# Performance work log

Hardware: AMD Instinct MI355X
Metric: run time of the kernel (lower is better)

Reference implementation:

```python
import jax, jax.numpy as jnp
import numpy as np

ALPHA = 1.0  # initial_alpha; forward uses self.alpha which stays at init value

def setup_inputs() -> dict:
    key = jax.random.key(0)
    k1, k2, k3, k4 = jax.random.split(key, 4)
    B, T, N, C, K = 8, 32, 2048, 64, 32
    R_seq = jax.random.normal(k1, (B, T, N, C), dtype=jnp.float32)
    W = jax.random.normal(k2, (K, C), dtype=jnp.float32) * (1.0 / np.sqrt(C))
    b = jax.random.normal(k3, (K,), dtype=jnp.float32) * 0.01
    cent = jax.random.normal(k4, (K, C), dtype=jnp.float32)
    centroids = cent / jnp.linalg.norm(cent, axis=1, keepdims=True)  # xavier + L2-normalize rows
    return {"R_seq": R_seq, "W": W, "b": b, "centroids": centroids}

def reference(R_seq, W, b, centroids):
    B, T, N, C = R_seq.shape
    K = centroids.shape[0]
    r = R_seq.reshape(B * T, N, C)                       # (BT, N, C)
    logits = (jnp.einsum('mnc,kc->mnk', r, W) + b) * ALPHA
    a = jax.nn.softmax(logits, axis=-1)                  # (BT, N, K)
    # NetVLAD algebraic decomposition: v_k = a_k^T r - (sum_n a_nk) * c_k
    v = jnp.einsum('mnk,mnc->mkc', a, r) - a.sum(axis=1)[:, :, None] * centroids[None]
    return v.reshape(B, T, K, C)
```

## Files before the change

### kernel.cpp

```cpp
#include <hip/hip_runtime.h>
#include <stdint.h>

typedef __attribute__((ext_vector_type(8))) short bf16x8;
typedef __attribute__((ext_vector_type(4))) short bf16x4;
typedef __attribute__((ext_vector_type(4))) float f32x4;

#define WAVES 8
#define R_STRIDE 72
#define A_STRIDE 40
#define R_LDS_SHORTS (32 * R_STRIDE)
#define A_LDS_SHORTS (32 * A_STRIDE)
#define WAVE_LDS (R_LDS_SHORTS + A_LDS_SHORTS)
#define VB_STRIDE 68

static __device__ __forceinline__ unsigned short f2bf(float f) {
    union { float f; unsigned int i; } x; x.f = f;
    unsigned int i = x.i;
    return (unsigned short)((i + 0x7FFFu + ((i >> 16) & 1u)) >> 16);
}

static __device__ __forceinline__ bf16x8 cvt8(float4 a, float4 b) {
    bf16x8 r;
    r[0] = (short)f2bf(a.x); r[1] = (short)f2bf(a.y);
    r[2] = (short)f2bf(a.z); r[3] = (short)f2bf(a.w);
    r[4] = (short)f2bf(b.x); r[5] = (short)f2bf(b.y);
    r[6] = (short)f2bf(b.z); r[7] = (short)f2bf(b.w);
    return r;
}

static __device__ __forceinline__ float row_sum16(float x) {
    union fi { float f; int i; };
    fi a, b; a.f = x;
    b.i = __builtin_amdgcn_mov_dpp(a.i, 0x128, 0xf, 0xf, false); a.f += b.f;
    b.i = __builtin_amdgcn_mov_dpp(a.i, 0x124, 0xf, 0xf, false); a.f += b.f;
    b.i = __builtin_amdgcn_mov_dpp(a.i, 0x122, 0xf, 0xf, false); a.f += b.f;
    b.i = __builtin_amdgcn_mov_dpp(a.i, 0x121, 0xf, 0xf, false); a.f += b.f;
    return a.f;
}


__global__ __launch_bounds__(512, 2)
void netvlad_fused(const float* __restrict__ R,
                   const float* __restrict__ W,
                   const float* __restrict__ bias,
                   const float* __restrict__ cent,
                   float* __restrict__ out)
{
    __shared__ short smem[WAVES * WAVE_LDS];
    __shared__ float suma_buf[4][32];

    const int tid  = threadIdx.x;
    const int wave = tid >> 6;
    const int lane = tid & 63;
    const int l15  = lane & 15;
    const int quad = lane >> 4;
    const int m    = blockIdx.x;

    short* r_lds = smem + wave * WAVE_LDS;
    short* a_lds = r_lds + R_LDS_SHORTS;

    const float* Rm = R + (size_t)m * (2048 * 64);

    bf16x8 wf[2][2];
#pragma unroll
    for (int kt = 0; kt < 2; ++kt)
#pragma unroll
        for (int cc = 0; cc < 2; ++cc) {
            const float* wp = W + (kt*16 + l15)*64 + cc*32 + quad*8;
            wf[kt][cc] = cvt8(*(const float4*)wp, *(const float4*)(wp + 4));
        }

    float bval[2];
    bval[0] = bias[l15];
    bval[1] = bias[16 + l15];

    f32x4 acc[2][4];
#pragma unroll
    for (int kt = 0; kt < 2; ++kt)
#pragma unroll
        for (int ct = 0; ct < 4; ++ct)
            acc[kt][ct] = (f32x4){0.f, 0.f, 0.f, 0.f};
    float suma[2] = {0.f, 0.f};

    float4 cur[2][2][2];
#pragma unroll
    for (int s = 0; s < 2; ++s)
#pragma unroll
        for (int cc = 0; cc < 2; ++cc) {
            const float* rp = Rm + (size_t)(wave*32 + s*16 + l15)*64 + cc*32 + quad*8;
            cur[s][cc][0] = *(const float4*)rp;
            cur[s][cc][1] = *(const float4*)(rp + 4);
        }

#pragma unroll
    for (int it = 0; it < 8; ++it) {
        float4 nxt[2][2][2];
        if (it < 7) {
            const int n0n = ((it+1)*WAVES + wave) * 32;
#pragma unroll
            for (int s = 0; s < 2; ++s)
#pragma unroll
                for (int cc = 0; cc < 2; ++cc) {
                    const float* rp = Rm + (size_t)(n0n + s*16 + l15)*64 + cc*32 + quad*8;
                    nxt[s][cc][0] = *(const float4*)rp;
                    nxt[s][cc][1] = *(const float4*)(rp + 4);
                }
        }

        bf16x8 af[2][2];
#pragma unroll
        for (int s = 0; s < 2; ++s) {
            const int g = (s*2 + (l15 >> 3)) & 3;
#pragma unroll
            for (int cc = 0; cc < 2; ++cc) {
                af[s][cc] = cvt8(cur[s][cc][0], cur[s][cc][1]);
                const int c0s = (cc*32 + quad*8) ^ (g << 4);
                *(bf16x8*)(r_lds + (s*16 + l15)*R_STRIDE + c0s) = af[s][cc];
            }
        }

        f32x4 d1[2][2];
#pragma unroll
        for (int s = 0; s < 2; ++s)
#pragma unroll
            for (int kt = 0; kt < 2; ++kt) {
                f32x4 d = (f32x4){0.f, 0.f, 0.f, 0.f};
                d = __builtin_amdgcn_mfma_f32_16x16x32_bf16(af[s][0], wf[kt][0], d, 0, 0, 0);
                d = __builtin_amdgcn_mfma_f32_16x16x32_bf16(af[s][1], wf[kt][1], d, 0, 0, 0);
                d1[s][kt] = d;
            }

#pragma unroll
        for (int s = 0; s < 2; ++s) {
            bf16x4 p0, p1;
            float a0s = 0.f, a1s = 0.f;
#pragma unroll
            for (int r = 0; r < 4; ++r) {
                float l0 = d1[s][0][r] + bval[0];
                float l1 = d1[s][1][r] + bval[1];
                float e0 = __expf(l0);
                float e1 = __expf(l1);
                float ss = row_sum16(e0 + e1);
                float rs = __builtin_amdgcn_rcpf(ss);
                float a0 = e0 * rs, a1 = e1 * rs;
                a0s += a0; a1s += a1;
                p0[r] = (short)f2bf(a0);
                p1[r] = (short)f2bf(a1);
            }
            suma[0] += a0s; suma[1] += a1s;
            *(bf16x4*)(a_lds + l15*A_STRIDE        + s*16 + quad*4) = p0;
            *(bf16x4*)(a_lds + (16 + l15)*A_STRIDE + s*16 + quad*4) = p1;
        }

        bf16x8 a2[2];
#pragma unroll
        for (int kt = 0; kt < 2; ++kt)
            a2[kt] = *(bf16x8*)(a_lds + (kt*16 + l15)*A_STRIDE + quad*8);

#pragma unroll
        for (int ct = 0; ct < 4; ++ct) {
            const short* bp = r_lds + (quad*8)*R_STRIDE + ((ct ^ quad) << 4) + l15;
            bf16x8 b2;
#pragma unroll
            for (int j = 0; j < 8; ++j)
                b2[j] = bp[j*R_STRIDE];
#pragma unroll
            for (int kt = 0; kt < 2; ++kt)
                acc[kt][ct] = __builtin_amdgcn_mfma_f32_16x16x32_bf16(a2[kt], b2, acc[kt][ct], 0, 0, 0);
        }

        if (it < 7) {
#pragma unroll
            for (int s = 0; s < 2; ++s)
#pragma unroll
                for (int cc = 0; cc < 2; ++cc) {
                    cur[s][cc][0] = nxt[s][cc][0];
                    cur[s][cc][1] = nxt[s][cc][1];
                }
        }
    }

#pragma unroll
    for (int kt = 0; kt < 2; ++kt) {
        suma[kt] += __shfl_xor(suma[kt], 16);
        suma[kt] += __shfl_xor(suma[kt], 32);
    }

    float* vbuf = (float*)smem;
    __syncthreads();
#pragma unroll
    for (int step = 4; step >= 1; step >>= 1) {
        if (wave >= step && wave < 2*step) {
            float* dst = vbuf + (wave - step) * (32 * VB_STRIDE);
#pragma unroll
            for (int kt = 0; kt < 2; ++kt)
#pragma unroll
                for (int ct = 0; ct < 4; ++ct)
#pragma unroll
                    for (int r = 0; r < 4; ++r)
                        dst[(kt*16 + quad*4 + r)*VB_STRIDE + ct*16 + l15] = acc[kt][ct][r];
            if (lane < 16) {
                suma_buf[wave - step][lane]      = suma[0];
                suma_buf[wave - step][lane + 16] = suma[1];
            }
        }
        __syncthreads();
        if (wave < step) {
            const float* src = vbuf + wave * (32 * VB_STRIDE);
#pragma unroll
            for (int kt = 0; kt < 2; ++kt)
#pragma unroll
                for (int ct = 0; ct < 4; ++ct)
#pragma unroll
                    for (int r = 0; r < 4; ++r)
                        acc[kt][ct][r] += src[(kt*16 + quad*4 + r)*VB_STRIDE + ct*16 + l15];
            suma[0] += suma_buf[wave][l15];
            suma[1] += suma_buf[wave][l15 + 16];
        }
        __syncthreads();
    }

    if (wave == 0) {
        float* op = out + (size_t)m * (32*64);
#pragma unroll
        for (int kt = 0; kt < 2; ++kt) {
#pragma unroll
            for (int r = 0; r < 4; ++r) {
                const int k = kt*16 + quad*4 + r;
                const float su = __shfl(suma[kt], quad*4 + r);
#pragma unroll
                for (int ct = 0; ct < 4; ++ct) {
                    const int c = ct*16 + l15;
                    const float cv = cent[k*64 + c];
                    op[k*64 + c] = acc[kt][ct][r] - su * cv;
                }
            }
        }
    }
}

extern "C" void kernel_launch(void* const* d_in, const int* in_sizes, int n_in,
                              void* d_out, int out_size, void* d_ws, size_t ws_size,
                              hipStream_t stream) {
    (void)in_sizes; (void)n_in; (void)out_size; (void)d_ws; (void)ws_size;
    const float* R = (const float*)d_in[0];
    const float* W = (const float*)d_in[1];
    const float* b = (const float*)d_in[2];
    const float* c = (const float*)d_in[3];
    float* out = (float*)d_out;

    hipLaunchKernelGGL(netvlad_fused, dim3(256), dim3(512), 0, stream, R, W, b, c, out);
}
```

Measured before the change: 202.1 us.

## Split N across four blocks with LDS DMA staging and atomic output

Each (B·T) slice's 2048 rows are now split across four 256-thread blocks, launching 1024 blocks instead of 256. Partial VLAD results are combined with atomicAdd into an output that a memset zeroes beforehand. The second GEMM now reads R through global_load_lds DMA into double-buffered fp32 LDS stages, converting to bf16 on read. The first GEMM still loads the same rows into registers, so R is fetched twice and relies on cache hits. The goal is more parallelism and better latency hiding on a memory-bound kernel, at the cost of an extra memset launch, atomic traffic and the duplicate R reads.

```diff
diff --git a/kernel.cpp b/kernel.cpp
--- a/kernel.cpp
+++ b/kernel.cpp
@@ -5,12 +5,11 @@
 typedef __attribute__((ext_vector_type(4))) short bf16x4;
 typedef __attribute__((ext_vector_type(4))) float f32x4;
 
-#define WAVES 8
-#define R_STRIDE 72
+#define NSPLIT 4
+#define WAVES 4
+#define STAGES 8
+#define STAGE_FLOATS (16 * 64)
 #define A_STRIDE 40
-#define R_LDS_SHORTS (32 * R_STRIDE)
-#define A_LDS_SHORTS (32 * A_STRIDE)
-#define WAVE_LDS (R_LDS_SHORTS + A_LDS_SHORTS)
 #define VB_STRIDE 68
 
 static __device__ __forceinline__ unsigned short f2bf(float f) {
@@ -38,28 +37,37 @@
     return a.f;
 }
 
-
-__global__ __launch_bounds__(512, 2)
+static __device__ __forceinline__ void dma16(const float* g, float* l) {
+    __builtin_amdgcn_global_load_lds(
+        (const __attribute__((address_space(1))) void*)g,
+        (__attribute__((address_space(3))) void*)l, 16, 0, 0);
+}
+
+__global__ __launch_bounds__(256, 3)
 void netvlad_fused(const float* __restrict__ R,
                    const float* __restrict__ W,
                    const float* __restrict__ bias,
                    const float* __restrict__ cent,
                    float* __restrict__ out)
 {
-    __shared__ short smem[WAVES * WAVE_LDS];
-    __shared__ float suma_buf[4][32];
+    __shared__ float dma[WAVES][2][STAGE_FLOATS];
+    __shared__ short a_lds_s[WAVES][32 * A_STRIDE];
+    __shared__ float suma_buf[2][32];
 
     const int tid  = threadIdx.x;
     const int wave = tid >> 6;
     const int lane = tid & 63;
     const int l15  = lane & 15;
     const int quad = lane >> 4;
-    const int m    = blockIdx.x;
-
-    short* r_lds = smem + wave * WAVE_LDS;
-    short* a_lds = r_lds + R_LDS_SHORTS;
-
-    const float* Rm = R + (size_t)m * (2048 * 64);
+    const int m    = blockIdx.x >> 2;
+    const int q    = blockIdx.x & 3;
+
+    const float* Rm  = R + (size_t)m * (2048 * 64);
+    const int row0   = q * 512 + wave * 128;
+
+    short* a_lds = a_lds_s[wave];
+    float* buf0  = dma[wave][0];
+    float* buf1  = dma[wave][1];
 
     bf16x8 wf[2][2];
 #pragma unroll
@@ -69,7 +77,6 @@
             const float* wp = W + (kt*16 + l15)*64 + cc*32 + quad*8;
             wf[kt][cc] = cvt8(*(const float4*)wp, *(const float4*)(wp + 4));
         }
-
     float bval[2];
     bval[0] = bias[l15];
     bval[1] = bias[16 + l15];
@@ -82,101 +89,94 @@
             acc[kt][ct] = (f32x4){0.f, 0.f, 0.f, 0.f};
     float suma[2] = {0.f, 0.f};
 
-    float4 cur[2][2][2];
-#pragma unroll
-    for (int s = 0; s < 2; ++s)
-#pragma unroll
-        for (int cc = 0; cc < 2; ++cc) {
-            const float* rp = Rm + (size_t)(wave*32 + s*16 + l15)*64 + cc*32 + quad*8;
-            cur[s][cc][0] = *(const float4*)rp;
-            cur[s][cc][1] = *(const float4*)(rp + 4);
-        }
-
-#pragma unroll
-    for (int it = 0; it < 8; ++it) {
-        float4 nxt[2][2][2];
-        if (it < 7) {
-            const int n0n = ((it+1)*WAVES + wave) * 32;
-#pragma unroll
-            for (int s = 0; s < 2; ++s)
-#pragma unroll
-                for (int cc = 0; cc < 2; ++cc) {
-                    const float* rp = Rm + (size_t)(n0n + s*16 + l15)*64 + cc*32 + quad*8;
-                    nxt[s][cc][0] = *(const float4*)rp;
-                    nxt[s][cc][1] = *(const float4*)(rp + 4);
-                }
-        }
-
-        bf16x8 af[2][2];
-#pragma unroll
-        for (int s = 0; s < 2; ++s) {
-            const int g = (s*2 + (l15 >> 3)) & 3;
-#pragma unroll
-            for (int cc = 0; cc < 2; ++cc) {
-                af[s][cc] = cvt8(cur[s][cc][0], cur[s][cc][1]);
-                const int c0s = (cc*32 + quad*8) ^ (g << 4);
-                *(bf16x8*)(r_lds + (s*16 + l15)*R_STRIDE + c0s) = af[s][cc];
+    {
+        const float* src = Rm + (size_t)row0 * 64;
+#pragma unroll
+        for (int t = 0; t < 4; ++t)
+            dma16(src + t*256 + lane*4, buf0 + t*256);
+    }
+    float4 cur[4];
+    {
+        const float* p = Rm + (size_t)row0*64 + l15*64 + quad*8;
+        cur[0] = *(const float4*)p;        cur[1] = *(const float4*)(p + 4);
+        cur[2] = *(const float4*)(p + 32); cur[3] = *(const float4*)(p + 36);
+    }
+
+#pragma unroll
+    for (int s = 0; s < STAGES; ++s) {
+        float* bufn = (s & 1) ? buf0 : buf1;
+        const float* nsrc = Rm + (size_t)(row0 + (s+1)*16) * 64;
+
+        if (!(s & 1) && s + 1 < STAGES) {
+#pragma unroll
+            for (int t = 0; t < 4; ++t)
+                dma16(nsrc + t*256 + lane*4, bufn + t*256);
+        }
+        float4 nxt[4];
+        if (s + 1 < STAGES) {
+            const float* p = nsrc + l15*64 + quad*8;
+            nxt[0] = *(const float4*)p;        nxt[1] = *(const float4*)(p + 4);
+            nxt[2] = *(const float4*)(p + 32); nxt[3] = *(const float4*)(p + 36);
+        }
+
+        bf16x8 af0 = cvt8(cur[0], cur[1]);
+        bf16x8 af1 = cvt8(cur[2], cur[3]);
+        f32x4 d1[2];
+#pragma unroll
+        for (int kt = 0; kt < 2; ++kt) {
+            f32x4 d = (f32x4){0.f, 0.f, 0.f, 0.f};
+            d = __builtin_amdgcn_mfma_f32_16x16x32_bf16(af0, wf[kt][0], d, 0, 0, 0);
+            d = __builtin_amdgcn_mfma_f32_16x16x32_bf16(af1, wf[kt][1], d, 0, 0, 0);
+            d1[kt] = d;
+        }
+
+        bf16x4 p0, p1;
+        float a0s = 0.f, a1s = 0.f;
+#pragma unroll
+        for (int r = 0; r < 4; ++r) {
+            float l0 = d1[0][r] + bval[0];
+            float l1 = d1[1][r] + bval[1];
+            float e0 = __expf(l0);
+            float e1 = __expf(l1);
+            float ss = row_sum16(e0 + e1);
+            float rs = __builtin_amdgcn_rcpf(ss);
+            float a0 = e0 * rs, a1 = e1 * rs;
+            a0s += a0; a1s += a1;
+            p0[r] = (short)f2bf(a0);
+            p1[r] = (short)f2bf(a1);
+        }
+        suma[0] += a0s; suma[1] += a1s;
+        *(bf16x4*)(a_lds + l15*A_STRIDE        + (s&1)*16 + quad*4) = p0;
+        *(bf16x4*)(a_lds + (16 + l15)*A_STRIDE + (s&1)*16 + quad*4) = p1;
+
+        if (s & 1) {
+            asm volatile("s_waitcnt vmcnt(4)" ::: "memory");
+
+            bf16x8 a2[2];
+            a2[0] = *(bf16x8*)(a_lds + l15*A_STRIDE        + quad*8);
+            a2[1] = *(bf16x8*)(a_lds + (16 + l15)*A_STRIDE + quad*8);
+
+            const float* bb = (quad < 2) ? buf0 : buf1;
+            const float* bp = bb + (quad & 1) * 8 * 64 + l15;
+#pragma unroll
+            for (int ct = 0; ct < 4; ++ct) {
+                const float* bq = bp + ct*16;
+                bf16x8 b2;
+#pragma unroll
+                for (int j = 0; j < 8; ++j)
+                    b2[j] = (short)f2bf(bq[j*64]);
+                acc[0][ct] = __builtin_amdgcn_mfma_f32_16x16x32_bf16(a2[0], b2, acc[0][ct], 0, 0, 0);
+                acc[1][ct] = __builtin_amdgcn_mfma_f32_16x16x32_bf16(a2[1], b2, acc[1][ct], 0, 0, 0);
             }
-        }
-
-        f32x4 d1[2][2];
-#pragma unroll
-        for (int s = 0; s < 2; ++s)
-#pragma unroll
-            for (int kt = 0; kt < 2; ++kt) {
-                f32x4 d = (f32x4){0.f, 0.f, 0.f, 0.f};
-                d = __builtin_amdgcn_mfma_f32_16x16x32_bf16(af[s][0], wf[kt][0], d, 0, 0, 0);
-                d = __builtin_amdgcn_mfma_f32_16x16x32_bf16(af[s][1], wf[kt][1], d, 0, 0, 0);
-                d1[s][kt] = d;
+            if (s + 1 < STAGES) {
+#pragma unroll
+                for (int t = 0; t < 4; ++t)
+                    dma16(nsrc + t*256 + lane*4, bufn + t*256);
             }
-
-#pragma unroll
-        for (int s = 0; s < 2; ++s) {
-            bf16x4 p0, p1;
-            float a0s = 0.f, a1s = 0.f;
-#pragma unroll
-            for (int r = 0; r < 4; ++r) {
-                float l0 = d1[s][0][r] + bval[0];
-                float l1 = d1[s][1][r] + bval[1];
-                float e0 = __expf(l0);
-                float e1 = __expf(l1);
-                float ss = row_sum16(e0 + e1);
-                float rs = __builtin_amdgcn_rcpf(ss);
-                float a0 = e0 * rs, a1 = e1 * rs;
-                a0s += a0; a1s += a1;
-                p0[r] = (short)f2bf(a0);
-                p1[r] = (short)f2bf(a1);
-            }
-            suma[0] += a0s; suma[1] += a1s;
-            *(bf16x4*)(a_lds + l15*A_STRIDE        + s*16 + quad*4) = p0;
-            *(bf16x4*)(a_lds + (16 + l15)*A_STRIDE + s*16 + quad*4) = p1;
-        }
-
-        bf16x8 a2[2];
-#pragma unroll
-        for (int kt = 0; kt < 2; ++kt)
-            a2[kt] = *(bf16x8*)(a_lds + (kt*16 + l15)*A_STRIDE + quad*8);
-
-#pragma unroll
-        for (int ct = 0; ct < 4; ++ct) {
-            const short* bp = r_lds + (quad*8)*R_STRIDE + ((ct ^ quad) << 4) + l15;
-            bf16x8 b2;
-#pragma unroll
-            for (int j = 0; j < 8; ++j)
-                b2[j] = bp[j*R_STRIDE];
-#pragma unroll
-            for (int kt = 0; kt < 2; ++kt)
-                acc[kt][ct] = __builtin_amdgcn_mfma_f32_16x16x32_bf16(a2[kt], b2, acc[kt][ct], 0, 0, 0);
-        }
-
-        if (it < 7) {
-#pragma unroll
-            for (int s = 0; s < 2; ++s)
-#pragma unroll
-                for (int cc = 0; cc < 2; ++cc) {
-                    cur[s][cc][0] = nxt[s][cc][0];
-                    cur[s][cc][1] = nxt[s][cc][1];
-                }
+        }
+
+        if (s + 1 < STAGES) {
+            cur[0] = nxt[0]; cur[1] = nxt[1]; cur[2] = nxt[2]; cur[3] = nxt[3];
         }
     }
 
@@ -186,41 +186,61 @@
         suma[kt] += __shfl_xor(suma[kt], 32);
     }
 
-    float* vbuf = (float*)smem;
-    __syncthreads();
-#pragma unroll
-    for (int step = 4; step >= 1; step >>= 1) {
-        if (wave >= step && wave < 2*step) {
-            float* dst = vbuf + (wave - step) * (32 * VB_STRIDE);
-#pragma unroll
-            for (int kt = 0; kt < 2; ++kt)
-#pragma unroll
-                for (int ct = 0; ct < 4; ++ct)
-#pragma unroll
-                    for (int r = 0; r < 4; ++r)
-                        dst[(kt*16 + quad*4 + r)*VB_STRIDE + ct*16 + l15] = acc[kt][ct][r];
-            if (lane < 16) {
-                suma_buf[wave - step][lane]      = suma[0];
-                suma_buf[wave - step][lane + 16] = suma[1];
-            }
-        }
-        __syncthreads();
-        if (wave < step) {
-            const float* src = vbuf + wave * (32 * VB_STRIDE);
-#pragma unroll
-            for (int kt = 0; kt < 2; ++kt)
-#pragma unroll
-                for (int ct = 0; ct < 4; ++ct)
-#pragma unroll
-                    for (int r = 0; r < 4; ++r)
-                        acc[kt][ct][r] += src[(kt*16 + quad*4 + r)*VB_STRIDE + ct*16 + l15];
-            suma[0] += suma_buf[wave][l15];
-            suma[1] += suma_buf[wave][l15 + 16];
-        }
-        __syncthreads();
-    }
-
+    float* vbuf = (float*)dma;
+    __syncthreads();
+    if (wave >= 2) {
+        float* dst = vbuf + (wave - 2) * (32 * VB_STRIDE);
+#pragma unroll
+        for (int kt = 0; kt < 2; ++kt)
+#pragma unroll
+            for (int ct = 0; ct < 4; ++ct)
+#pragma unroll
+                for (int r = 0; r < 4; ++r)
+                    dst[(kt*16 + quad*4 + r)*VB_STRIDE + ct*16 + l15] = acc[kt][ct][r];
+        if (lane < 16) {
+            suma_buf[wave - 2][lane]      = suma[0];
+            suma_buf[wave - 2][lane + 16] = suma[1];
+        }
+    }
+    __syncthreads();
+    if (wave < 2) {
+        const float* src = vbuf + wave * (32 * VB_STRIDE);
+#pragma unroll
+        for (int kt = 0; kt < 2; ++kt)
+#pragma unroll
+            for (int ct = 0; ct < 4; ++ct)
+#pragma unroll
+                for (int r = 0; r < 4; ++r)
+                    acc[kt][ct][r] += src[(kt*16 + quad*4 + r)*VB_STRIDE + ct*16 + l15];
+        suma[0] += suma_buf[wave][l15];
+        suma[1] += suma_buf[wave][l15 + 16];
+    }
+    __syncthreads();
+    if (wave == 1) {
+#pragma unroll
+        for (int kt = 0; kt < 2; ++kt)
+#pragma unroll
+            for (int ct = 0; ct < 4; ++ct)
+#pragma unroll
+                for (int r = 0; r < 4; ++r)
+                    vbuf[(kt*16 + quad*4 + r)*VB_STRIDE + ct*16 + l15] = acc[kt][ct][r];
+        if (lane < 16) {
+            suma_buf[0][lane]      = suma[0];
+            suma_buf[0][lane + 16] = suma[1];
+        }
+    }
+    __syncthreads();
     if (wave == 0) {
+#pragma unroll
+        for (int kt = 0; kt < 2; ++kt)
+#pragma unroll
+            for (int ct = 0; ct < 4; ++ct)
+#pragma unroll
+                for (int r = 0; r < 4; ++r)
+                    acc[kt][ct][r] += vbuf[(kt*16 + quad*4 + r)*VB_STRIDE + ct*16 + l15];
+        suma[0] += suma_buf[0][l15];
+        suma[1] += suma_buf[0][l15 + 16];
+
         float* op = out + (size_t)m * (32*64);
 #pragma unroll
         for (int kt = 0; kt < 2; ++kt) {
@@ -231,8 +251,7 @@
 #pragma unroll
                 for (int ct = 0; ct < 4; ++ct) {
                     const int c = ct*16 + l15;
-                    const float cv = cent[k*64 + c];
-                    op[k*64 + c] = acc[kt][ct][r] - su * cv;
+                    atomicAdd(&op[k*64 + c], acc[kt][ct][r] - su * cent[k*64 + c]);
                 }
             }
         }
@@ -249,5 +268,7 @@
     const float* c = (const float*)d_in[3];
     float* out = (float*)d_out;
 
-    hipLaunchKernelGGL(netvlad_fused, dim3(256), dim3(512), 0, stream, R, W, b, c, out);
-}
+    hipMemsetAsync(out, 0, (size_t)256 * 32 * 64 * sizeof(float), stream);
+    hipLaunchKernelGGL(netvlad_fused, dim3(256 * NSPLIT), dim3(256), 0, stream,
+                       R, W, b, c, out);
+}
```

Result: slower. 216.8 us (+7.3%).
